# Kernel optimization log

Hardware: AMD Instinct MI355X
Metric: run time of the kernel (lower is better)

Reference implementation:

```python
import jax, jax.numpy as jnp
import numpy as np

DIAG_MASK = 1e20  # value added on the diagonal to exclude self as negative


def setup_inputs() -> dict:
    key = jax.random.key(0)
    k1, k2, k3 = jax.random.split(key, 3)
    B, D_in, D_out = 4096, 1024, 1024
    anchor_x = jax.random.normal(k1, (B, D_in), dtype=jnp.float32)
    pos_x = jax.random.normal(k2, (B, D_in), dtype=jnp.float32)
    W = jax.random.normal(k3, (D_in, D_out), dtype=jnp.float32) * (1.0 / np.sqrt(D_in))
    b = jnp.zeros((D_out,), dtype=jnp.float32)
    return {"anchor_x": anchor_x, "pos_x": pos_x, "W": W, "b": b}


def reference(anchor_x, pos_x, W, b):
    # Encoder: simple dense projection (stand-in for the wrapped BERT encoder).
    anchor = anchor_x @ W + b          # [B, D]
    pos = pos_x @ W + b                # [B, D]

    # Pairwise squared distances dist[i,j] = ||anchor_i - pos_j||^2,
    # computed via the GEMM identity |a|^2 + |p|^2 - 2 a.p (same math as the
    # original broadcasted (a_i - p_j)^2 reduce_sum, far less memory traffic).
    a2 = jnp.sum(anchor * anchor, axis=-1, keepdims=True)       # [B, 1]
    p2 = jnp.sum(pos * pos, axis=-1, keepdims=True).T           # [1, B]
    dist = a2 + p2 - 2.0 * (anchor @ pos.T)                     # [B, B]

    B = dist.shape[0]
    mask_dist = dist + jnp.eye(B, dtype=dist.dtype) * DIAG_MASK  # mask diagonal
    indices = jnp.argmin(mask_dist, axis=-1)                     # [B] hard negatives
    neg = pos[indices]                                           # gather [B, D]

    return jnp.concatenate([anchor, pos, neg], axis=-1)          # [B, 3D]
```

## Files before the change

### kernel.cpp

```cpp
#include <hip/hip_runtime.h>


typedef short s8v __attribute__((ext_vector_type(8)));
typedef _Float16 h8v __attribute__((ext_vector_type(8)));
typedef float f4v __attribute__((ext_vector_type(4)));
typedef unsigned short u16;

#define B  4096
#define D  1024
#define OLD 3072
#define OLD16 6144
#define LDK 68

__device__ __forceinline__ u16 f2bf(float f) {
  union { float f; unsigned u; } v; v.f = f;
  unsigned r = v.u + 0x7FFFu + ((v.u >> 16) & 1u);
  return (u16)(r >> 16);
}
__device__ __forceinline__ float bf2f(u16 s) {
  union { unsigned u; float f; } v; v.u = ((unsigned)s) << 16;
  return v.f;
}

__device__ __forceinline__ void gld16(const void* g, void* l) {
  __builtin_amdgcn_global_load_lds(
      (const __attribute__((address_space(1))) unsigned int*)g,
      (__attribute__((address_space(3))) unsigned int*)l, 16, 0, 0);
}

struct Top2 { float v1, v2; int j1, j2; };
__device__ __forceinline__ void t2_insert(Top2& t, float v, int j) {
  if (v < t.v1 || (v == t.v1 && j < t.j1)) {
    t.v2 = t.v1; t.j2 = t.j1; t.v1 = v; t.j1 = j;
  } else if (v < t.v2 || (v == t.v2 && j < t.j2)) {
    t.v2 = v; t.j2 = j;
  }
}
struct Top4 { float v[4]; int j[4]; };
__device__ __forceinline__ void t4_insert(Top4& t, float v, int j) {
  if (v < t.v[3] || (v == t.v[3] && j < t.j[3])) {
    int p = 3;
#pragma unroll
    for (int s = 0; s < 3; ++s) {
      if (p > 0 && (v < t.v[p - 1] || (v == t.v[p - 1] && j < t.j[p - 1]))) {
        t.v[p] = t.v[p - 1]; t.j[p] = t.j[p - 1]; --p;
      }
    }
    t.v[p] = v; t.j[p] = j;
  }
}

__global__ void splitT_W(const float* __restrict__ W, u16* __restrict__ WtQ) {
  __shared__ float tile[32][33];
  const int bx = blockIdx.x * 32, by = blockIdx.y * 32;
  const int tx = threadIdx.x, ty = threadIdx.y;
  for (int dy = 0; dy < 32; dy += 8)
    tile[ty + dy][tx] = W[(size_t)(by + ty + dy) * D + bx + tx];
  __syncthreads();
  for (int dy = 0; dy < 32; dy += 8) {
    const float v = tile[tx][ty + dy];
    const u16 h = f2bf(v);
    const size_t o = (size_t)(bx + ty + dy) * 2048 + by + tx;
    WtQ[o] = h;
    WtQ[o + 1024] = f2bf(v - bf2f(h));
  }
}

__global__ __launch_bounds__(256) void splitX2(
    const float* __restrict__ A, const float* __restrict__ P,
    u16* __restrict__ O16, u16* __restrict__ posXq) {
  const int r = blockIdx.x, t = threadIdx.x;
  const bool isPos = r >= B;
  const int row = isPos ? r - B : r;
  const float4 v = *(const float4*)&(isPos ? P : A)[(size_t)row * D + t * 4];
  const float vv[4] = {v.x, v.y, v.z, v.w};
  ushort4 hi, mi;
  u16* hp = &hi.x; u16* mp = &mi.x;
#pragma unroll
  for (int i = 0; i < 4; ++i) {
    hp[i] = f2bf(vv[i]);
    mp[i] = f2bf(vv[i] - bf2f(hp[i]));
  }
  if (isPos) {
    *(ushort4*)&posXq[(size_t)row * 2048 + t * 4] = hi;
    *(ushort4*)&posXq[(size_t)row * 2048 + 1024 + t * 4] = mi;
  } else {
    *(ushort4*)&O16[(size_t)row * OLD16 + 4096 + t * 4] = hi;
    *(ushort4*)&O16[(size_t)row * OLD16 + 5120 + t * 4] = mi;
  }
}

__global__ __launch_bounds__(256) void enc_mfma(
    float* out, const u16* __restrict__ posXq, const u16* __restrict__ WtQ,
    const float* __restrict__ bias, _Float16* __restrict__ Aq,
    _Float16* __restrict__ Pq) {
  __shared__ __align__(16) u16 lAh[128 * 32], lAm[128 * 32];
  __shared__ __align__(16) u16 lBh[128 * 32], lBm[128 * 32];
  const u16* O16 = (const u16*)out;
  const int tid = threadIdx.x, lane = tid & 63, wave = tid >> 6;
  const int waveM = wave >> 1, waveN = wave & 1;
  const int row16 = lane & 15, quad = lane >> 4;
  const bool isPos = blockIdx.y >= 32;
  const int Mbase = (blockIdx.y & 31) * 128;
  const int Nbase = blockIdx.x * 128;
  f4v acc[4][4] = {};
  const int slot = (quad ^ ((row16 >> 1) & 3)) * 8;

  for (int kk = 0; kk < D; kk += 32) {
    __syncthreads();
#pragma unroll
    for (int i = 0; i < 2; ++i) {
      const int c = i * 256 + tid;
      const int row = c >> 2;
      const int col8 = ((c & 3) ^ ((row >> 1) & 3)) * 8;
      const int lo = (i * 256 + wave * 64) * 8;
      if (isPos) {
        gld16(&posXq[(size_t)(Mbase + row) * 2048 + kk + col8], &lAh[lo]);
        gld16(&posXq[(size_t)(Mbase + row) * 2048 + 1024 + kk + col8], &lAm[lo]);
      } else {
        gld16(&O16[(size_t)(Mbase + row) * OLD16 + 4096 + kk + col8], &lAh[lo]);
        gld16(&O16[(size_t)(Mbase + row) * OLD16 + 5120 + kk + col8], &lAm[lo]);
      }
      gld16(&WtQ[(size_t)(Nbase + row) * 2048 + kk + col8], &lBh[lo]);
      gld16(&WtQ[(size_t)(Nbase + row) * 2048 + 1024 + kk + col8], &lBm[lo]);
    }
    __syncthreads();
    s8v ah[4], am[4], bh[4], bm[4];
#pragma unroll
    for (int mi = 0; mi < 4; ++mi) {
      const int ro = (waveM * 64 + mi * 16 + row16) * 32 + slot;
      ah[mi] = *(const s8v*)&lAh[ro];
      am[mi] = *(const s8v*)&lAm[ro];
    }
#pragma unroll
    for (int ni = 0; ni < 4; ++ni) {
      const int ro = (waveN * 64 + ni * 16 + row16) * 32 + slot;
      bh[ni] = *(const s8v*)&lBh[ro];
      bm[ni] = *(const s8v*)&lBm[ro];
    }
#pragma unroll
    for (int mi = 0; mi < 4; ++mi)
#pragma unroll
      for (int ni = 0; ni < 4; ++ni) {
        f4v a = acc[mi][ni];
        a = __builtin_amdgcn_mfma_f32_16x16x32_bf16(ah[mi], bh[ni], a, 0, 0, 0);
        a = __builtin_amdgcn_mfma_f32_16x16x32_bf16(ah[mi], bm[ni], a, 0, 0, 0);
        a = __builtin_amdgcn_mfma_f32_16x16x32_bf16(am[mi], bh[ni], a, 0, 0, 0);
        acc[mi][ni] = a;
      }
  }
  const int outOff = isPos ? 1024 : 0;
  _Float16* Q = isPos ? Pq : Aq;
#pragma unroll
  for (int ni = 0; ni < 4; ++ni) {
    const int col = Nbase + waveN * 64 + ni * 16 + row16;
    const float bv = bias[col];
#pragma unroll
    for (int mi = 0; mi < 4; ++mi) {
      const int rbase = Mbase + waveM * 64 + mi * 16 + quad * 4;
#pragma unroll
      for (int r = 0; r < 4; ++r) {
        const size_t row = rbase + r;
        const float v = acc[mi][ni][r] + bv;
        out[row * OLD + outOff + col] = v;
        Q[row * 1024 + col] = (_Float16)v;
      }
    }
  }
}

__global__ __launch_bounds__(256) void pnorm(float* __restrict__ o) {
  const int row = blockIdx.x, t = threadIdx.x;
  const float4 v = *(const float4*)&o[(size_t)row * OLD + D + t * 4];
  float s = v.x * v.x + v.y * v.y + v.z * v.z + v.w * v.w;
#pragma unroll
  for (int off = 32; off; off >>= 1) s += __shfl_down(s, off, 64);
  __shared__ float wsum[4];
  if ((t & 63) == 0) wsum[t >> 6] = s;
  __syncthreads();
  if (t == 0) o[(size_t)row * OLD + 2048] = wsum[0] + wsum[1] + wsum[2] + wsum[3];
}

__global__ __launch_bounds__(512, 2) void dist_mfma(
    const _Float16* __restrict__ Aq, const _Float16* __restrict__ Pq,
    float* __restrict__ o) {
  __shared__ __align__(16) u16 lA[4][256 * 32];
  __shared__ __align__(16) u16 lB[4][256 * 32];
  const int tid = threadIdx.x, lane = tid & 63, wave = tid >> 6;
  const int waveM = wave >> 2, waveN = wave & 3;
  const int row16 = lane & 15, quad = lane >> 4;
  const int Mbase = blockIdx.y * 256;
  const int Nbase = blockIdx.x * 256;
  f4v acc[8][4] = {};

  auto STAGE = [&](int buf, int kk) {
#pragma unroll
    for (int i = 0; i < 2; ++i) {
      const int c = i * 512 + tid;
      const int row = c >> 2;
      const int col8 = ((c & 3) ^ ((row >> 1) & 3)) * 8;
      u16* la = &lA[buf][(i * 512 + wave * 64) * 8];
      u16* lb = &lB[buf][(i * 512 + wave * 64) * 8];
      gld16(&Aq[(size_t)(Mbase + row) * 1024 + kk + col8], la);
      gld16(&Pq[(size_t)(Nbase + row) * 1024 + kk + col8], lb);
    }
  };

  STAGE(0, 0);
  STAGE(1, 32);
  const int slot = (quad ^ ((row16 >> 1) & 3)) * 8;
  for (int t = 0; t < 32; ++t) {
    if (t + 2 < 32) STAGE((t + 2) & 3, (t + 2) * 32);
    if (t < 30)       asm volatile("s_waitcnt vmcnt(8)" ::: "memory");
    else if (t == 30) asm volatile("s_waitcnt vmcnt(4)" ::: "memory");
    else              asm volatile("s_waitcnt vmcnt(0)" ::: "memory");
    __builtin_amdgcn_sched_barrier(0);
    __builtin_amdgcn_s_barrier();
    __builtin_amdgcn_sched_barrier(0);
    const int cur = t & 3;
    h8v a[8], b[4];
#pragma unroll
    for (int mi = 0; mi < 8; ++mi)
      a[mi] = *(const h8v*)&lA[cur][(waveM * 128 + mi * 16 + row16) * 32 + slot];
#pragma unroll
    for (int ni = 0; ni < 4; ++ni)
      b[ni] = *(const h8v*)&lB[cur][(waveN * 64 + ni * 16 + row16) * 32 + slot];
    __builtin_amdgcn_s_setprio(1);
#pragma unroll
    for (int mi = 0; mi < 8; ++mi)
#pragma unroll
      for (int ni = 0; ni < 4; ++ni)
        acc[mi][ni] =
            __builtin_amdgcn_mfma_f32_16x16x32_f16(a[mi], b[ni], acc[mi][ni], 0, 0, 0);
    __builtin_amdgcn_s_setprio(0);
  }
  __syncthreads();

  float (*sv1)[4] = (float(*)[4])&lA[0][0];
  float (*sv2)[4] = (float(*)[4])((char*)&lA[0][0] + 4096);
  int   (*sj1)[4] = (int(*)[4])((char*)&lA[0][0] + 8192);
  int   (*sj2)[4] = (int(*)[4])((char*)&lA[0][0] + 12288);

  float p2c[4];
#pragma unroll
  for (int ni = 0; ni < 4; ++ni)
    p2c[ni] = o[(size_t)(Nbase + waveN * 64 + ni * 16 + row16) * OLD + 2048];
#pragma unroll
  for (int mi = 0; mi < 8; ++mi)
#pragma unroll
    for (int r = 0; r < 4; ++r) {
      const int rg = Mbase + waveM * 128 + mi * 16 + quad * 4 + r;
      Top2 tp; tp.v1 = 3.0e38f; tp.v2 = 3.0e38f; tp.j1 = 0; tp.j2 = 1;
#pragma unroll
      for (int ni = 0; ni < 4; ++ni) {
        const int cg = Nbase + waveN * 64 + ni * 16 + row16;
        if (cg != rg) t2_insert(tp, p2c[ni] - 2.0f * acc[mi][ni][r], cg);
      }
#pragma unroll
      for (int m = 1; m < 16; m <<= 1) {
        const float ov1 = __shfl_xor(tp.v1, m, 64);
        const int oj1 = __shfl_xor(tp.j1, m, 64);
        const float ov2 = __shfl_xor(tp.v2, m, 64);
        const int oj2 = __shfl_xor(tp.j2, m, 64);
        t2_insert(tp, ov1, oj1);
        t2_insert(tp, ov2, oj2);
      }
      if (row16 == 0) {
        const int rl = waveM * 128 + mi * 16 + quad * 4 + r;
        sv1[rl][waveN] = tp.v1; sj1[rl][waveN] = tp.j1;
        sv2[rl][waveN] = tp.v2; sj2[rl][waveN] = tp.j2;
      }
    }
  __syncthreads();
  if (tid < 256) {
    Top2 tp; tp.v1 = sv1[tid][0]; tp.j1 = sj1[tid][0];
    tp.v2 = sv2[tid][0]; tp.j2 = sj2[tid][0];
#pragma unroll
    for (int w = 1; w < 4; ++w) {
      t2_insert(tp, sv1[tid][w], sj1[tid][w]);
      t2_insert(tp, sv2[tid][w], sj2[tid][w]);
    }
    ((float4*)&o[(size_t)(Mbase + tid) * OLD + 2056])[blockIdx.x] =
        make_float4(tp.v1, __int_as_float(tp.j1), tp.v2, __int_as_float(tp.j2));
  }
}

__global__ __launch_bounds__(256) void argmin_refine(float* __restrict__ o) {
  const int i = blockIdx.x, t = threadIdx.x;
  __shared__ int gj[4];
  if (t < 64) {
    Top4 tp;
#pragma unroll
    for (int c = 0; c < 4; ++c) { tp.v[c] = 3.0e38f; tp.j[c] = 0; }
    if (t < 16) {
      const float4 p = ((const float4*)&o[(size_t)i * OLD + 2056])[t];
      t4_insert(tp, p.x, __float_as_int(p.y));
      t4_insert(tp, p.z, __float_as_int(p.w));
    }
#pragma unroll
    for (int m = 1; m < 32; m <<= 1) {
#pragma unroll
      for (int c = 0; c < 4; ++c) {
        const float ov = __shfl_xor(tp.v[c], m, 64);
        const int oj = __shfl_xor(tp.j[c], m, 64);
        t4_insert(tp, ov, oj);
      }
    }
    if (t == 0) {
#pragma unroll
      for (int c = 0; c < 4; ++c)
        gj[c] = (tp.j[c] < 0) ? 0 : (tp.j[c] > B - 1 ? B - 1 : tp.j[c]);
    }
  }
  __syncthreads();
  int jj[4];
#pragma unroll
  for (int c = 0; c < 4; ++c) jj[c] = gj[c];
  const float4 a4 = *(const float4*)&o[(size_t)i * OLD + t * 4];
  float s[4], n[4];
#pragma unroll
  for (int c = 0; c < 4; ++c) {
    const float4 q = *(const float4*)&o[(size_t)jj[c] * OLD + D + t * 4];
    s[c] = a4.x * q.x + a4.y * q.y + a4.z * q.z + a4.w * q.w;
    n[c] = q.x * q.x + q.y * q.y + q.z * q.z + q.w * q.w;
  }
#pragma unroll
  for (int off = 32; off; off >>= 1)
#pragma unroll
    for (int c = 0; c < 4; ++c) {
      s[c] += __shfl_down(s[c], off, 64);
      n[c] += __shfl_down(n[c], off, 64);
    }
  __shared__ float wsum[4][8];
  __shared__ int sjf;
  if ((t & 63) == 0)
#pragma unroll
    for (int c = 0; c < 4; ++c) {
      wsum[t >> 6][c] = s[c];
      wsum[t >> 6][4 + c] = n[c];
    }
  __syncthreads();
  if (t == 0) {
    float bd = 3.4e38f; int bj = 0x7fffffff;
#pragma unroll
    for (int c = 0; c < 4; ++c) {
      const float S = wsum[0][c] + wsum[1][c] + wsum[2][c] + wsum[3][c];
      const float N = wsum[0][4 + c] + wsum[1][4 + c] + wsum[2][4 + c] + wsum[3][4 + c];
      const float d = N - 2.0f * S;
      const int j = jj[c];
      if (d < bd || (d == bd && j < bj)) { bd = d; bj = j; }
    }
    sjf = bj;
  }
  __syncthreads();
  const int j = sjf;
  ((float4*)&o[(size_t)i * OLD + 2048])[t] = ((const float4*)&o[(size_t)j * OLD + D])[t];
}

__global__ __launch_bounds__(256) void enc_gemm(
    const float* __restrict__ X, const float* __restrict__ W,
    const float* __restrict__ bia, float* __restrict__ out, int outOff) {
  __shared__ float lA[32][LDK];
  __shared__ float lW[32][LDK];
  const int tid = threadIdx.x;
  const int Mbase = blockIdx.y * 64;
  const int Nbase = blockIdx.x * 64;
  const int ty = tid >> 4, tx = tid & 15;
  float acc[4][4] = {};
  for (int k0 = 0; k0 < D; k0 += 32) {
    __syncthreads();
#pragma unroll
    for (int h = 0; h < 2; ++h) {
      const int ch = tid + h * 256;
      const int r = ch >> 3, c4 = (ch & 7) * 4;
      const float4 a4 = *(const float4*)&X[(size_t)(Mbase + r) * D + k0 + c4];
      lA[c4 + 0][r] = a4.x; lA[c4 + 1][r] = a4.y;
      lA[c4 + 2][r] = a4.z; lA[c4 + 3][r] = a4.w;
      const int kr = ch >> 4, nc = (ch & 15) * 4;
      *(float4*)&lW[kr][nc] = *(const float4*)&W[(size_t)(k0 + kr) * D + Nbase + nc];
    }
    __syncthreads();
#pragma unroll
    for (int kk = 0; kk < 32; ++kk) {
      const float4 av = *(const float4*)&lA[kk][ty * 4];
      const float4 wv = *(const float4*)&lW[kk][tx * 4];
      acc[0][0] += av.x * wv.x; acc[0][1] += av.x * wv.y; acc[0][2] += av.x * wv.z; acc[0][3] += av.x * wv.w;
      acc[1][0] += av.y * wv.x; acc[1][1] += av.y * wv.y; acc[1][2] += av.y * wv.z; acc[1][3] += av.y * wv.w;
      acc[2][0] += av.z * wv.x; acc[2][1] += av.z * wv.y; acc[2][2] += av.z * wv.z; acc[2][3] += av.z * wv.w;
      acc[3][0] += av.w * wv.x; acc[3][1] += av.w * wv.y; acc[3][2] += av.w * wv.z; acc[3][3] += av.w * wv.w;
    }
  }
  const float4 b4 = *(const float4*)&bia[Nbase + tx * 4];
#pragma unroll
  for (int i = 0; i < 4; ++i) {
    const int row = Mbase + ty * 4 + i;
    float4 ov;
    ov.x = acc[i][0] + b4.x; ov.y = acc[i][1] + b4.y;
    ov.z = acc[i][2] + b4.z; ov.w = acc[i][3] + b4.w;
    *(float4*)&out[(size_t)row * OLD + outOff + Nbase + tx * 4] = ov;
  }
}

__global__ __launch_bounds__(256) void dist_argmin_f32(float* __restrict__ o) {
  __shared__ float lA[32][LDK];
  __shared__ float lB[32][LDK];
  const int tid = threadIdx.x;
  const int Mbase = blockIdx.y * 64, Nbase = blockIdx.x * 64;
  const int ty = tid >> 4, tx = tid & 15;
  float acc[4][4] = {};
  for (int k0 = 0; k0 < D; k0 += 32) {
    __syncthreads();
#pragma unroll
    for (int h = 0; h < 2; ++h) {
      const int ch = tid + h * 256;
      const int r = ch >> 3, c4 = (ch & 7) * 4;
      const float4 a4 = *(const float4*)&o[(size_t)(Mbase + r) * OLD + k0 + c4];
      const float4 b4 = *(const float4*)&o[(size_t)(Nbase + r) * OLD + D + k0 + c4];
      lA[c4 + 0][r] = a4.x; lA[c4 + 1][r] = a4.y;
      lA[c4 + 2][r] = a4.z; lA[c4 + 3][r] = a4.w;
      lB[c4 + 0][r] = b4.x; lB[c4 + 1][r] = b4.y;
      lB[c4 + 2][r] = b4.z; lB[c4 + 3][r] = b4.w;
    }
    __syncthreads();
#pragma unroll
    for (int kk = 0; kk < 32; ++kk) {
      const float4 av = *(const float4*)&lA[kk][ty * 4];
      const float4 bv = *(const float4*)&lB[kk][tx * 4];
      acc[0][0] += av.x * bv.x; acc[0][1] += av.x * bv.y; acc[0][2] += av.x * bv.z; acc[0][3] += av.x * bv.w;
      acc[1][0] += av.y * bv.x; acc[1][1] += av.y * bv.y; acc[1][2] += av.y * bv.z; acc[1][3] += av.y * bv.w;
      acc[2][0] += av.z * bv.x; acc[2][1] += av.z * bv.y; acc[2][2] += av.z * bv.z; acc[2][3] += av.z * bv.w;
      acc[3][0] += av.w * bv.x; acc[3][1] += av.w * bv.y; acc[3][2] += av.w * bv.z; acc[3][3] += av.w * bv.w;
    }
  }
  float colp2[4];
#pragma unroll
  for (int j = 0; j < 4; ++j)
    colp2[j] = o[(size_t)(Nbase + tx * 4 + j) * OLD + 2048];
#pragma unroll
  for (int i = 0; i < 4; ++i) {
    const int rg = Mbase + ty * 4 + i;
    float bv = 3.0e38f; int bj = 0;
#pragma unroll
    for (int j = 0; j < 4; ++j) {
      const int cg = Nbase + tx * 4 + j;
      const float d = colp2[j] - 2.0f * acc[i][j];
      if (cg != rg && d < bv) { bv = d; bj = cg; }
    }
#pragma unroll
    for (int m = 1; m < 16; m <<= 1) {
      const float ov = __shfl_xor(bv, m, 64);
      const int oj = __shfl_xor(bj, m, 64);
      if (ov < bv || (ov == bv && oj < bj)) { bv = ov; bj = oj; }
    }
    if (tx == 0)
      ((float2*)&o[(size_t)rg * OLD + 2056])[blockIdx.x] =
          make_float2(bv, __int_as_float(bj));
  }
}

__global__ __launch_bounds__(256) void argmin_final_f2(float* __restrict__ o, int nblk) {
  const int i = blockIdx.x, t = threadIdx.x;
  __shared__ int sj;
  if (t < 64) {
    float v = 3.4e38f; int j = 0x7fffffff;
    if (t < nblk) {
      const float2 p = ((const float2*)&o[(size_t)i * OLD + 2056])[t];
      v = p.x; j = __float_as_int(p.y);
    }
#pragma unroll
    for (int m = 32; m; m >>= 1) {
      const float ov = __shfl_xor(v, m, 64);
      const int oj = __shfl_xor(j, m, 64);
      if (ov < v || (ov == v && oj < j)) { v = ov; j = oj; }
    }
    if (t == 0) sj = (j < 0) ? 0 : (j > B - 1 ? B - 1 : j);
  }
  __syncthreads();
  const int j = sj;
  ((float4*)&o[(size_t)i * OLD + 2048])[t] = ((const float4*)&o[(size_t)j * OLD + D])[t];
}

extern "C" void kernel_launch(void* const* d_in, const int* in_sizes, int n_in,
                              void* d_out, int out_size, void* d_ws, size_t ws_size,
                              hipStream_t stream) {
  const float* anchor_x = (const float*)d_in[0];
  const float* pos_x    = (const float*)d_in[1];
  const float* W        = (const float*)d_in[2];
  const float* b        = (const float*)d_in[3];
  float* out = (float*)d_out;
  char* ws = (char*)d_ws;
  const size_t MB = 1024 * 1024;

  if (ws_size >= 36 * MB) {
    _Float16* Aq = (_Float16*)(ws);
    _Float16* Pq = (_Float16*)(ws + 8 * MB);
    u16* WtQ     = (u16*)(ws + 16 * MB);
    u16* posXq   = (u16*)(ws + 20 * MB);
    splitT_W<<<dim3(32, 32), dim3(32, 8), 0, stream>>>(W, WtQ);
    splitX2<<<2 * B, 256, 0, stream>>>(anchor_x, pos_x, (u16*)out, posXq);
    enc_mfma<<<dim3(8, 64), 256, 0, stream>>>(out, posXq, WtQ, b, Aq, Pq);
    pnorm<<<B, 256, 0, stream>>>(out);
    dist_mfma<<<dim3(16, 16), 512, 0, stream>>>(Aq, Pq, out);
    argmin_refine<<<B, 256, 0, stream>>>(out);
  } else {
    enc_gemm<<<dim3(16, 64), 256, 0, stream>>>(anchor_x, W, b, out, 0);
    enc_gemm<<<dim3(16, 64), 256, 0, stream>>>(pos_x,    W, b, out, 1024);
    pnorm<<<B, 256, 0, stream>>>(out);
    dist_argmin_f32<<<dim3(64, 64), 256, 0, stream>>>(out);
    argmin_final_f2<<<B, 256, 0, stream>>>(out, 64);
  }
}
```

Before: 288.4 us.

## Pipeline encoder GEMM global-to-LDS loads with 4-buffer prefetch depth two

Restructures the encoder MFMA loop so each K tile is loaded into one of four LDS buffers two iterations ahead, using explicit vmcnt waits and a single barrier per iteration instead of two. This hides global load latency behind the MFMA work. It also raises wave priority around the MFMA block. LDS use grows fourfold (to 128KB per block), which may lower occupancy.

```diff
diff --git a/kernel.cpp b/kernel.cpp
--- a/kernel.cpp
+++ b/kernel.cpp
@@ -94,8 +94,8 @@
     float* out, const u16* __restrict__ posXq, const u16* __restrict__ WtQ,
     const float* __restrict__ bias, _Float16* __restrict__ Aq,
     _Float16* __restrict__ Pq) {
-  __shared__ __align__(16) u16 lAh[128 * 32], lAm[128 * 32];
-  __shared__ __align__(16) u16 lBh[128 * 32], lBm[128 * 32];
+  __shared__ __align__(16) u16 lAh[4][128 * 32], lAm[4][128 * 32];
+  __shared__ __align__(16) u16 lBh[4][128 * 32], lBm[4][128 * 32];
   const u16* O16 = (const u16*)out;
   const int tid = threadIdx.x, lane = tid & 63, wave = tid >> 6;
   const int waveM = wave >> 1, waveN = wave & 1;
@@ -106,8 +106,7 @@
   f4v acc[4][4] = {};
   const int slot = (quad ^ ((row16 >> 1) & 3)) * 8;
 
-  for (int kk = 0; kk < D; kk += 32) {
-    __syncthreads();
+  auto STAGE = [&](int buf, int kk) {
 #pragma unroll
     for (int i = 0; i < 2; ++i) {
       const int c = i * 256 + tid;
@@ -115,29 +114,42 @@
       const int col8 = ((c & 3) ^ ((row >> 1) & 3)) * 8;
       const int lo = (i * 256 + wave * 64) * 8;
       if (isPos) {
-        gld16(&posXq[(size_t)(Mbase + row) * 2048 + kk + col8], &lAh[lo]);
-        gld16(&posXq[(size_t)(Mbase + row) * 2048 + 1024 + kk + col8], &lAm[lo]);
+        gld16(&posXq[(size_t)(Mbase + row) * 2048 + kk + col8], &lAh[buf][lo]);
+        gld16(&posXq[(size_t)(Mbase + row) * 2048 + 1024 + kk + col8], &lAm[buf][lo]);
       } else {
-        gld16(&O16[(size_t)(Mbase + row) * OLD16 + 4096 + kk + col8], &lAh[lo]);
-        gld16(&O16[(size_t)(Mbase + row) * OLD16 + 5120 + kk + col8], &lAm[lo]);
-      }
-      gld16(&WtQ[(size_t)(Nbase + row) * 2048 + kk + col8], &lBh[lo]);
-      gld16(&WtQ[(size_t)(Nbase + row) * 2048 + 1024 + kk + col8], &lBm[lo]);
-    }
-    __syncthreads();
+        gld16(&O16[(size_t)(Mbase + row) * OLD16 + 4096 + kk + col8], &lAh[buf][lo]);
+        gld16(&O16[(size_t)(Mbase + row) * OLD16 + 5120 + kk + col8], &lAm[buf][lo]);
+      }
+      gld16(&WtQ[(size_t)(Nbase + row) * 2048 + kk + col8], &lBh[buf][lo]);
+      gld16(&WtQ[(size_t)(Nbase + row) * 2048 + 1024 + kk + col8], &lBm[buf][lo]);
+    }
+  };
+
+  STAGE(0, 0);
+  STAGE(1, 32);
+  for (int t = 0; t < 32; ++t) {
+    if (t + 2 < 32) STAGE((t + 2) & 3, (t + 2) * 32);
+    if (t < 30)       asm volatile("s_waitcnt vmcnt(16)" ::: "memory");
+    else if (t == 30) asm volatile("s_waitcnt vmcnt(8)" ::: "memory");
+    else              asm volatile("s_waitcnt vmcnt(0)" ::: "memory");
+    __builtin_amdgcn_sched_barrier(0);
+    __builtin_amdgcn_s_barrier();
+    __builtin_amdgcn_sched_barrier(0);
+    const int cur = t & 3;
     s8v ah[4], am[4], bh[4], bm[4];
 #pragma unroll
     for (int mi = 0; mi < 4; ++mi) {
       const int ro = (waveM * 64 + mi * 16 + row16) * 32 + slot;
-      ah[mi] = *(const s8v*)&lAh[ro];
-      am[mi] = *(const s8v*)&lAm[ro];
+      ah[mi] = *(const s8v*)&lAh[cur][ro];
+      am[mi] = *(const s8v*)&lAm[cur][ro];
     }
 #pragma unroll
     for (int ni = 0; ni < 4; ++ni) {
       const int ro = (waveN * 64 + ni * 16 + row16) * 32 + slot;
-      bh[ni] = *(const s8v*)&lBh[ro];
-      bm[ni] = *(const s8v*)&lBm[ro];
-    }
+      bh[ni] = *(const s8v*)&lBh[cur][ro];
+      bm[ni] = *(const s8v*)&lBm[cur][ro];
+    }
+    __builtin_amdgcn_s_setprio(1);
 #pragma unroll
     for (int mi = 0; mi < 4; ++mi)
 #pragma unroll
@@ -148,6 +160,7 @@
         a = __builtin_amdgcn_mfma_f32_16x16x32_bf16(am[mi], bh[ni], a, 0, 0, 0);
         acc[mi][ni] = a;
       }
+    __builtin_amdgcn_s_setprio(0);
   }
   const int outOff = isPos ? 1024 : 0;
   _Float16* Q = isPos ? Pq : Aq;
```

Measured after the change: 294.4 us. 2.1% more time.
